# Performance work log

Hardware: AMD Instinct MI355X
Metric: run time of the kernel (lower is better)

The kernel has to match this reference:

```python
import jax, jax.numpy as jnp
import numpy as np

ALPHA = 5.0
EPS = 1e-12  # avoids inf grad of sqrt at the self-distance (exact 0)


def setup_inputs() -> dict:
    key = jax.random.key(0)
    xyz = jax.random.normal(key, (4, 8192, 3), dtype=jnp.float32)
    return {"xyz": xyz, "nbr_size": 2}


def reference(xyz, nbr_size):
    # Brute-force KNN of xyz against itself (self is included with dist 0,
    # matching pointops.knn(query, ref) when query == ref).
    sq = jnp.sum(xyz * xyz, axis=-1)                      # (B, N)
    # squared pairwise distances: ||a||^2 + ||b||^2 - 2 a.b  -> (B, N, N)
    d2 = sq[:, :, None] + sq[:, None, :] - 2.0 * jnp.einsum(
        'bnd,bmd->bnm', xyz, xyz)
    neg_top, _idx = jax.lax.top_k(-d2, nbr_size)          # (B, N, k) smallest d2
    dist = jnp.sqrt(jnp.maximum(-neg_top, EPS))           # Euclidean distance
    dsum = dist.sum(-1)                                   # (B, N)
    avg_dist = dsum.mean(-1, keepdims=True)               # (B, 1)
    # loss = sum of per-point distance sums exceeding alpha * mean
    loss = jnp.where(dsum > avg_dist * ALPHA, dsum, 0.0).sum()
    return loss
```

## Files before the change

kernel.cpp:

```cpp
#include <hip/hip_runtime.h>

#define BB 4
#define NN 8192
#define BN (BB * NN)
#define ALPHA 5.0f
#define EPSF 1e-12f
#define BLOCK 256
#define QPT 4
#define QB (BLOCK * QPT)
#define BIGF 1e30f

template <int NSEG>
__global__ __launch_bounds__(BLOCK, 8) void knn_kernel(
    const float* __restrict__ xyz, float2* __restrict__ pairs) {
  constexpr int SEG = NN / NSEG;
  constexpr int CHUNKS = NN / QB;
  int bid = blockIdx.x;
  int s = bid % NSEG;
  int rem = bid / NSEG;
  int qchunk = rem % CHUNKS;
  int b = rem / CHUNKS;

  const float* xb = xyz + (size_t)b * NN * 3;

  __shared__ float4 tile[SEG];
  int refBase = s * SEG;
  for (int r0 = threadIdx.x; r0 < SEG; r0 += BLOCK) {
    int r = refBase + r0;
    float px = xb[3 * r + 0], py = xb[3 * r + 1], pz = xb[3 * r + 2];
    float hpp = 0.5f * fmaf(px, px, fmaf(py, py, pz * pz));
    tile[r0] = make_float4(px, py, pz, hpp);
  }

  float nqx[QPT], nqy[QPT], nqz[QPT], hq[QPT], m1[QPT], m2[QPT];
#pragma unroll
  for (int i = 0; i < QPT; i++) {
    int q = qchunk * QB + threadIdx.x + i * BLOCK;
    float x = xb[3 * q + 0], y = xb[3 * q + 1], z = xb[3 * q + 2];
    nqx[i] = -x;
    nqy[i] = -y;
    nqz[i] = -z;
    hq[i] = 0.5f * fmaf(x, x, fmaf(y, y, z * z));
    m1[i] = BIGF;
    m2[i] = BIGF;
  }
  __syncthreads();

#pragma unroll 4
  for (int j = 0; j < SEG; j++) {
    float4 p = tile[j];
#pragma unroll
    for (int i = 0; i < QPT; i++) {
      float t = fmaf(nqx[i], p.x, p.w);
      t = fmaf(nqy[i], p.y, t);
      t = fmaf(nqz[i], p.z, t);
      float d = hq[i] + t;
      float nm2 = __builtin_amdgcn_fmed3f(d, m1[i], m2[i]);
      m1[i] = fminf(m1[i], d);
      m2[i] = nm2;
    }
  }

#pragma unroll
  for (int i = 0; i < QPT; i++) {
    int q = qchunk * QB + threadIdx.x + i * BLOCK;
    pairs[(size_t)s * BN + b * NN + q] = make_float2(m1[i], m2[i]);
  }
}

template <int NSEG>
__global__ __launch_bounds__(BLOCK) void merge_kernel(
    const float2* __restrict__ pairs, float* __restrict__ dsum,
    float* __restrict__ partial) {
  int g = blockIdx.x * BLOCK + threadIdx.x;
  float m1 = BIGF, m2 = BIGF;
#pragma unroll 8
  for (int s = 0; s < NSEG; s++) {
    float2 p = pairs[(size_t)s * BN + g];
    float n2 = __builtin_amdgcn_fmed3f(p.x, m1, m2);
    m1 = fminf(m1, p.x);
    m2 = n2;
    n2 = __builtin_amdgcn_fmed3f(p.y, m1, m2);
    m1 = fminf(m1, p.y);
    m2 = n2;
  }
  float ds = sqrtf(fmaxf(m1 + m1, EPSF)) + sqrtf(fmaxf(m2 + m2, EPSF));
  dsum[g] = ds;

  float v = ds;
#pragma unroll
  for (int off = 32; off > 0; off >>= 1) v += __shfl_down(v, off, 64);
  __shared__ float warp_sums[BLOCK / 64];
  if ((threadIdx.x & 63) == 0) warp_sums[threadIdx.x >> 6] = v;
  __syncthreads();
  if (threadIdx.x == 0) {
    float t = 0.0f;
#pragma unroll
    for (int w = 0; w < BLOCK / 64; w++) t += warp_sums[w];
    partial[blockIdx.x] = t;
  }
}

#define LBLK 1024
#define NPART (BN / BLOCK)
__global__ __launch_bounds__(LBLK) void loss_kernel(
    const float* __restrict__ dsum, const float* __restrict__ partial,
    float* __restrict__ out) {
  __shared__ float s_avg[BB];
  if (threadIdx.x < NPART) {
    float v = partial[threadIdx.x];
#pragma unroll
    for (int off = 16; off > 0; off >>= 1) v += __shfl_down(v, off, 32);
    if ((threadIdx.x & 31) == 0) s_avg[threadIdx.x >> 5] = v * (ALPHA / NN);
  }
  __syncthreads();

  const float4* d4 = (const float4*)dsum;
  float acc = 0.0f;
#pragma unroll
  for (int it = 0; it < BN / (LBLK * 4); it++) {
    int idx = it * LBLK + threadIdx.x;
    float4 v = d4[idx];
    float thr = s_avg[idx >> 11];
    acc += (v.x > thr) ? v.x : 0.0f;
    acc += (v.y > thr) ? v.y : 0.0f;
    acc += (v.z > thr) ? v.z : 0.0f;
    acc += (v.w > thr) ? v.w : 0.0f;
  }
#pragma unroll
  for (int off = 32; off > 0; off >>= 1) acc += __shfl_down(acc, off, 64);
  __shared__ float warp_sums[LBLK / 64];
  if ((threadIdx.x & 63) == 0) warp_sums[threadIdx.x >> 6] = acc;
  __syncthreads();
  if (threadIdx.x == 0) {
    float t = 0.0f;
#pragma unroll
    for (int w = 0; w < LBLK / 64; w++) t += warp_sums[w];
    out[0] = t;
  }
}

template <int NSEG>
static void run(const float* xyz, float* out, void* d_ws, hipStream_t stream) {
  float2* pairs = (float2*)d_ws;
  float* dsum = (float*)(pairs + (size_t)NSEG * BN);
  float* partial = dsum + BN;
  int grid1 = BB * (NN / QB) * NSEG;
  knn_kernel<NSEG><<<grid1, BLOCK, 0, stream>>>(xyz, pairs);
  merge_kernel<NSEG><<<BN / BLOCK, BLOCK, 0, stream>>>(pairs, dsum, partial);
  loss_kernel<<<1, LBLK, 0, stream>>>(dsum, partial, out);
}

extern "C" void kernel_launch(void* const* d_in, const int* in_sizes, int n_in,
                              void* d_out, int out_size, void* d_ws,
                              size_t ws_size, hipStream_t stream) {
  const float* xyz = (const float*)d_in[0];
  float* out = (float*)d_out;

  auto need = [](int nseg) {
    return (size_t)nseg * BN * sizeof(float2) + BN * sizeof(float) +
           NPART * sizeof(float);
  };
  if (ws_size >= need(64)) {
    run<64>(xyz, out, d_ws, stream);
  } else if (ws_size >= need(32)) {
    run<32>(xyz, out, d_ws, stream);
  } else {
    run<16>(xyz, out, d_ws, stream);
  }
}
```

Measured before the change: 100.7 us.

## Precompute packed float4 refs and read them directly from global in KNN

Adds a prep kernel that packs xyz plus half squared norm into float4. The KNN kernel then reads reference points straight from global memory, which are uniform loads likely served by scalar or cache paths, instead of staging a shared tile, and the __syncthreads goes away. The query norm term is added once after the loop rather than on every candidate, and the merge block size shrinks to 128. The segment count drops to 32 or lower, so each block does more work per reference, at the cost of an extra kernel launch and extra workspace.

```diff
diff --git a/kernel.cpp b/kernel.cpp
--- a/kernel.cpp
+++ b/kernel.cpp
@@ -10,9 +10,17 @@
 #define QB (BLOCK * QPT)
 #define BIGF 1e30f
 
+__global__ __launch_bounds__(BLOCK) void prep_kernel(
+    const float* __restrict__ xyz, float4* __restrict__ refs4) {
+  int g = blockIdx.x * BLOCK + threadIdx.x;
+  float x = xyz[3 * g + 0], y = xyz[3 * g + 1], z = xyz[3 * g + 2];
+  float hpp = 0.5f * fmaf(x, x, fmaf(y, y, z * z));
+  refs4[g] = make_float4(x, y, z, hpp);
+}
+
 template <int NSEG>
 __global__ __launch_bounds__(BLOCK, 8) void knn_kernel(
-    const float* __restrict__ xyz, float2* __restrict__ pairs) {
+    const float4* __restrict__ refs4, float2* __restrict__ pairs) {
   constexpr int SEG = NN / NSEG;
   constexpr int CHUNKS = NN / QB;
   int bid = blockIdx.x;
@@ -21,58 +29,51 @@
   int qchunk = rem % CHUNKS;
   int b = rem / CHUNKS;
 
-  const float* xb = xyz + (size_t)b * NN * 3;
-
-  __shared__ float4 tile[SEG];
-  int refBase = s * SEG;
-  for (int r0 = threadIdx.x; r0 < SEG; r0 += BLOCK) {
-    int r = refBase + r0;
-    float px = xb[3 * r + 0], py = xb[3 * r + 1], pz = xb[3 * r + 2];
-    float hpp = 0.5f * fmaf(px, px, fmaf(py, py, pz * pz));
-    tile[r0] = make_float4(px, py, pz, hpp);
-  }
+  const float4* __restrict__ qb4 = refs4 + (size_t)b * NN;
 
   float nqx[QPT], nqy[QPT], nqz[QPT], hq[QPT], m1[QPT], m2[QPT];
 #pragma unroll
   for (int i = 0; i < QPT; i++) {
     int q = qchunk * QB + threadIdx.x + i * BLOCK;
-    float x = xb[3 * q + 0], y = xb[3 * q + 1], z = xb[3 * q + 2];
-    nqx[i] = -x;
-    nqy[i] = -y;
-    nqz[i] = -z;
-    hq[i] = 0.5f * fmaf(x, x, fmaf(y, y, z * z));
+    float4 qp = qb4[q];
+    nqx[i] = -qp.x;
+    nqy[i] = -qp.y;
+    nqz[i] = -qp.z;
+    hq[i] = qp.w;
     m1[i] = BIGF;
     m2[i] = BIGF;
   }
-  __syncthreads();
 
+  const float4* __restrict__ rp = qb4 + s * SEG;
 #pragma unroll 4
   for (int j = 0; j < SEG; j++) {
-    float4 p = tile[j];
+    float4 p = rp[j];
+    float pw = p.w;
 #pragma unroll
     for (int i = 0; i < QPT; i++) {
-      float t = fmaf(nqx[i], p.x, p.w);
+      float t = fmaf(nqx[i], p.x, pw);
       t = fmaf(nqy[i], p.y, t);
       t = fmaf(nqz[i], p.z, t);
-      float d = hq[i] + t;
-      float nm2 = __builtin_amdgcn_fmed3f(d, m1[i], m2[i]);
-      m1[i] = fminf(m1[i], d);
-      m2[i] = nm2;
+      m2[i] = __builtin_amdgcn_fmed3f(t, m1[i], m2[i]);
+      m1[i] = fminf(m1[i], t);
     }
   }
 
 #pragma unroll
   for (int i = 0; i < QPT; i++) {
     int q = qchunk * QB + threadIdx.x + i * BLOCK;
-    pairs[(size_t)s * BN + b * NN + q] = make_float2(m1[i], m2[i]);
+    pairs[(size_t)s * BN + b * NN + q] =
+        make_float2(m1[i] + hq[i], m2[i] + hq[i]);
   }
 }
 
+#define MBLK 128
+#define NPART (BN / MBLK)
 template <int NSEG>
-__global__ __launch_bounds__(BLOCK) void merge_kernel(
+__global__ __launch_bounds__(MBLK) void merge_kernel(
     const float2* __restrict__ pairs, float* __restrict__ dsum,
     float* __restrict__ partial) {
-  int g = blockIdx.x * BLOCK + threadIdx.x;
+  int g = blockIdx.x * MBLK + threadIdx.x;
   float m1 = BIGF, m2 = BIGF;
 #pragma unroll 8
   for (int s = 0; s < NSEG; s++) {
@@ -90,19 +91,19 @@
   float v = ds;
 #pragma unroll
   for (int off = 32; off > 0; off >>= 1) v += __shfl_down(v, off, 64);
-  __shared__ float warp_sums[BLOCK / 64];
+  __shared__ float warp_sums[MBLK / 64];
   if ((threadIdx.x & 63) == 0) warp_sums[threadIdx.x >> 6] = v;
   __syncthreads();
   if (threadIdx.x == 0) {
     float t = 0.0f;
 #pragma unroll
-    for (int w = 0; w < BLOCK / 64; w++) t += warp_sums[w];
+    for (int w = 0; w < MBLK / 64; w++) t += warp_sums[w];
     partial[blockIdx.x] = t;
   }
 }
 
 #define LBLK 1024
-#define NPART (BN / BLOCK)
+#define PPB (NPART / BB)
 __global__ __launch_bounds__(LBLK) void loss_kernel(
     const float* __restrict__ dsum, const float* __restrict__ partial,
     float* __restrict__ out) {
@@ -110,8 +111,8 @@
   if (threadIdx.x < NPART) {
     float v = partial[threadIdx.x];
 #pragma unroll
-    for (int off = 16; off > 0; off >>= 1) v += __shfl_down(v, off, 32);
-    if ((threadIdx.x & 31) == 0) s_avg[threadIdx.x >> 5] = v * (ALPHA / NN);
+    for (int off = 32; off > 0; off >>= 1) v += __shfl_down(v, off, 64);
+    if ((threadIdx.x & 63) == 0) s_avg[threadIdx.x >> 6] = v * (ALPHA / NN);
   }
   __syncthreads();
 
@@ -143,11 +144,13 @@
 template <int NSEG>
 static void run(const float* xyz, float* out, void* d_ws, hipStream_t stream) {
   float2* pairs = (float2*)d_ws;
-  float* dsum = (float*)(pairs + (size_t)NSEG * BN);
+  float4* refs4 = (float4*)(pairs + (size_t)NSEG * BN);
+  float* dsum = (float*)(refs4 + BN);
   float* partial = dsum + BN;
+  prep_kernel<<<BN / BLOCK, BLOCK, 0, stream>>>(xyz, refs4);
   int grid1 = BB * (NN / QB) * NSEG;
-  knn_kernel<NSEG><<<grid1, BLOCK, 0, stream>>>(xyz, pairs);
-  merge_kernel<NSEG><<<BN / BLOCK, BLOCK, 0, stream>>>(pairs, dsum, partial);
+  knn_kernel<NSEG><<<grid1, BLOCK, 0, stream>>>(refs4, pairs);
+  merge_kernel<NSEG><<<BN / MBLK, MBLK, 0, stream>>>(pairs, dsum, partial);
   loss_kernel<<<1, LBLK, 0, stream>>>(dsum, partial, out);
 }
 
@@ -158,14 +161,14 @@
   float* out = (float*)d_out;
 
   auto need = [](int nseg) {
-    return (size_t)nseg * BN * sizeof(float2) + BN * sizeof(float) +
-           NPART * sizeof(float);
+    return (size_t)nseg * BN * sizeof(float2) + BN * sizeof(float4) +
+           BN * sizeof(float) + NPART * sizeof(float);
   };
-  if (ws_size >= need(64)) {
-    run<64>(xyz, out, d_ws, stream);
-  } else if (ws_size >= need(32)) {
+  if (ws_size >= need(32)) {
     run<32>(xyz, out, d_ws, stream);
+  } else if (ws_size >= need(16)) {
+    run<16>(xyz, out, d_ws, stream);
   } else {
-    run<16>(xyz, out, d_ws, stream);
+    run<8>(xyz, out, d_ws, stream);
   }
 }
```

Result: no change. 98.86 us (-1.8%).
